# Kernel tuning notes

Measured on AMD Instinct MI355X. Metric: run time of the kernel, lower is better.

Reference implementation:

```python
import jax, jax.numpy as jnp
import numpy as np

C = 256
C8 = C // 8
B, H, W = 4, 64, 64


def setup_inputs() -> dict:
    key = jax.random.key(0)
    ks = jax.random.split(key, 8)
    s = 0.05
    return {
        "x": jax.random.normal(ks[0], (B, C, H, W), jnp.float32),
        "wq": jax.random.normal(ks[1], (C8, C), jnp.float32) * s,
        "bq": jax.random.normal(ks[2], (C8,), jnp.float32) * s,
        "wk": jax.random.normal(ks[3], (C8, C), jnp.float32) * s,
        "bk": jax.random.normal(ks[4], (C8,), jnp.float32) * s,
        "wv": jax.random.normal(ks[5], (C, C), jnp.float32) * s,
        "bv": jax.random.normal(ks[6], (C,), jnp.float32) * s,
        "gamma": jax.random.normal(ks[7], (1,), jnp.float32),
    }


def reference(x, wq, bq, wk, bk, wv, bv, gamma):
    b, c, h, w = x.shape
    n = h * w
    xf = x.reshape(b, c, n)                                   # [B,C,N]
    # 1x1 convs == channel matmuls
    q = jnp.einsum('dc,bcn->bnd', wq, xf) + bq                # [B,N,C8] (query, permuted)
    k = jnp.einsum('dc,bcn->bdn', wk, xf) + bk[None, :, None]  # [B,C8,N]
    v = jnp.einsum('ec,bcn->ben', wv, xf) + bv[None, :, None]  # [B,C,N]
    # attention[b,i,j] = <q_i, k_j>, softmax over j (no scaling, as in source)
    attn = jax.nn.softmax(jnp.einsum('bnd,bdm->bnm', q, k), axis=-1)  # [B,N,N]
    # out = value @ attn^T : out[b,e,i] = sum_j v[b,e,j] * attn[b,i,j]
    out = jnp.einsum('bej,bij->bei', v, attn).reshape(b, c, h, w)
    return gamma * out + x
```

## Files before the change

kernel.cpp:

```cpp
#include <hip/hip_runtime.h>
#include <math.h>

typedef __attribute__((ext_vector_type(8))) short bf16x8;
typedef __attribute__((ext_vector_type(4))) float f32x4;
typedef unsigned short ushort;
typedef unsigned int uint;

#define F4(p)  (*reinterpret_cast<float4*>(p))
#define CF4(p) (*reinterpret_cast<const float4*>(p))

__device__ __forceinline__ ushort f2bf(float f) {
    uint u = __float_as_uint(f);
    return (ushort)((u + 0x7FFFu + ((u >> 16) & 1u)) >> 16);
}
__device__ __forceinline__ float bf2f(ushort h) {
    return __uint_as_float(((uint)h) << 16);
}

__global__ __launch_bounds__(256) void proj_kernel(
    const float* __restrict__ x,
    const float* __restrict__ wq, const float* __restrict__ bq,
    const float* __restrict__ wk, const float* __restrict__ bk,
    const float* __restrict__ wv, const float* __restrict__ bv,
    ushort* __restrict__ ws)
{
    ushort* qth = ws;
    ushort* qtl = qth + 524288;
    ushort* kth = qtl + 524288;
    ushort* ktl = kth + 524288;
    ushort* vhp = ktl + 524288;
    ushort* vlp = vhp + 4194304;

    __shared__ float Xt[64][260];
    __shared__ __align__(16) ushort Oh[4096];
    __shared__ __align__(16) ushort Ol[4096];

    const int t   = threadIdx.x;
    const int blk = blockIdx.x;
    const int b   = blk >> 6;
    const int n0  = (blk & 63) * 64;

    {
        const int tn4 = (t & 15) * 4;
        const int c0  = t >> 4;
        #pragma unroll
        for (int cc = 0; cc < 16; ++cc) {
            const int c = c0 + (cc << 4);
            const float4 xv = CF4(&x[(((size_t)b * 256 + c) << 12) + n0 + tn4]);
            Xt[tn4 + 0][c] = xv.x;
            Xt[tn4 + 1][c] = xv.y;
            Xt[tn4 + 2][c] = xv.z;
            Xt[tn4 + 3][c] = xv.w;
        }
    }
    __syncthreads();

    const int td = t >> 4;
    const int tn = t & 15;

    for (int g = 0; g < 5; ++g) {
        const int d0 = g * 64;
        float acc[4][4];
        #pragma unroll
        for (int i = 0; i < 4; ++i)
            #pragma unroll
            for (int j = 0; j < 4; ++j) acc[i][j] = 0.f;

        const float* wrow[4];
        float bias[4];
        #pragma unroll
        for (int dd = 0; dd < 4; ++dd) {
            const int rr = d0 + td + (dd << 4);
            if (rr < 32)      { wrow[dd] = wq + rr * 256;        bias[dd] = bq[rr]; }
            else if (rr < 64) { wrow[dd] = wk + (rr - 32) * 256; bias[dd] = bk[rr - 32]; }
            else              { wrow[dd] = wv + (rr - 64) * 256; bias[dd] = bv[rr - 64]; }
        }

        for (int c = 0; c < 256; c += 4) {
            float4 w4[4];
            #pragma unroll
            for (int dd = 0; dd < 4; ++dd) w4[dd] = CF4(&wrow[dd][c]);
            #pragma unroll
            for (int nn = 0; nn < 4; ++nn) {
                const float4 xv = CF4(&Xt[tn + (nn << 4)][c]);
                #pragma unroll
                for (int dd = 0; dd < 4; ++dd) {
                    acc[dd][nn] += w4[dd].x * xv.x + w4[dd].y * xv.y
                                 + w4[dd].z * xv.z + w4[dd].w * xv.w;
                }
            }
        }

        #pragma unroll
        for (int dd = 0; dd < 4; ++dd) {
            const int rr = d0 + td + (dd << 4);
            #pragma unroll
            for (int nn = 0; nn < 4; ++nn) {
                const int nl  = tn + (nn << 4);
                const float val = acc[dd][nn] + bias[dd];
                const ushort h  = f2bf(val);
                const ushort lo = f2bf(val - bf2f(h));
                int o;
                if (g == 0) o = (rr < 32) ? nl * 32 + rr : 2048 + nl * 32 + (rr - 32);
                else        o = (rr - d0) * 64 + nl;
                Oh[o] = h; Ol[o] = lo;
            }
        }
        __syncthreads();

        if (g == 0) {
            const size_t qb = ((size_t)(b * 4096 + n0)) * 32;
            #pragma unroll
            for (int s = 0; s < 2; ++s) {
                const int o = t * 16 + s * 8;
                const float4 vh = F4(&Oh[o]);
                const float4 vl = F4(&Ol[o]);
                if (o < 2048) {
                    F4(&qth[qb + o]) = vh;
                    F4(&qtl[qb + o]) = vl;
                } else {
                    F4(&kth[qb + o - 2048]) = vh;
                    F4(&ktl[qb + o - 2048]) = vl;
                }
            }
        } else {
            const size_t vb = ((size_t)(b * 256 + (g - 1) * 64)) * 4096 + n0;
            #pragma unroll
            for (int s = 0; s < 2; ++s) {
                const int o  = t * 16 + s * 8;
                const size_t ga = vb + (size_t)(o >> 6) * 4096 + (o & 63);
                F4(&vhp[ga]) = F4(&Oh[o]);
                F4(&vlp[ga]) = F4(&Ol[o]);
            }
        }
        __syncthreads();
    }
}

__global__ __launch_bounds__(256, 2) void attn_kernel(
    const ushort* __restrict__ ws,
    const float* __restrict__ x,
    const float* __restrict__ gamma,
    float* __restrict__ out)
{
    const ushort* qth = ws;
    const ushort* qtl = qth + 524288;
    const ushort* kth = qtl + 524288;
    const ushort* ktl = kth + 524288;
    const ushort* vhp = ktl + 524288;
    const ushort* vlp = vhp + 4194304;

    __shared__ __align__(16) ushort Ph[4096];
    __shared__ __align__(16) ushort Pl[4096];
    __shared__ float fac_sh[64];
    __shared__ float l_sh[64];

    const int t    = threadIdx.x;
    const int w    = t >> 6;
    const int lane = t & 63;
    const int m    = lane & 15;
    const int gr   = lane >> 4;

    const int blk = blockIdx.x;
    const int e8  = blk & 7;
    const int g_  = blk >> 3;
    const int b   = e8 >> 1;
    const int i0  = ((g_ & 31) + ((e8 & 1) << 5)) << 6;
    const int ebase = ((g_ >> 5) << 7) + w * 32;

    const size_t qkbase = (size_t)b * 4096 * 32;
    const size_t vbase  = (size_t)b * 256 * 4096;

    const int iq = i0 + w * 16 + m;
    const bf16x8 qbh = *(const bf16x8*)(qth + qkbase + (size_t)iq * 32 + 8 * gr);
    const bf16x8 qbl = *(const bf16x8*)(qtl + qkbase + (size_t)iq * 32 + 8 * gr);

    f32x4 accv[2][4];
    #pragma unroll
    for (int a = 0; a < 2; ++a)
        #pragma unroll
        for (int c = 0; c < 4; ++c) accv[a][c] = f32x4{0.f, 0.f, 0.f, 0.f};

    float m_run = -INFINITY, l_run = 0.f;
    const int irow = w * 16 + m;

    for (int jt = 0; jt < 64; ++jt) {
        const int j0 = jt << 6;

        bf16x8 kh[4], kl[4];
        #pragma unroll
        for (int mf = 0; mf < 4; ++mf) {
            const size_t ko = qkbase + (size_t)(j0 + mf * 16 + m) * 32 + 8 * gr;
            kh[mf] = *(const bf16x8*)(kth + ko);
            kl[mf] = *(const bf16x8*)(ktl + ko);
        }
        f32x4 st[4];
        #pragma unroll
        for (int mf = 0; mf < 4; ++mf) {
            f32x4 a = {0.f, 0.f, 0.f, 0.f};
            a = __builtin_amdgcn_mfma_f32_16x16x32_bf16(kh[mf], qbh, a, 0, 0, 0);
            a = __builtin_amdgcn_mfma_f32_16x16x32_bf16(kh[mf], qbl, a, 0, 0, 0);
            a = __builtin_amdgcn_mfma_f32_16x16x32_bf16(kl[mf], qbh, a, 0, 0, 0);
            st[mf] = a;
        }
        float tm = st[0][0];
        #pragma unroll
        for (int mf = 0; mf < 4; ++mf)
            #pragma unroll
            for (int r = 0; r < 4; ++r) tm = fmaxf(tm, st[mf][r]);
        tm = fmaxf(tm, __shfl_xor(tm, 16));
        tm = fmaxf(tm, __shfl_xor(tm, 32));
        const float m_new = fmaxf(m_run, tm);
        const float fac   = __expf(m_run - m_new);
        float p[4][4];
        float ts = 0.f;
        #pragma unroll
        for (int mf = 0; mf < 4; ++mf)
            #pragma unroll
            for (int r = 0; r < 4; ++r) {
                p[mf][r] = __expf(st[mf][r] - m_new);
                ts += p[mf][r];
            }
        ts += __shfl_xor(ts, 16);
        ts += __shfl_xor(ts, 32);
        l_run = l_run * fac + ts;
        m_run = m_new;

        #pragma unroll
        for (int mf = 0; mf < 4; ++mf) {
            const int j    = mf * 16 + 4 * gr;
            const int addr = irow * 64 + (j ^ ((irow & 7) << 3));
            ushort h0 = f2bf(p[mf][0]), h1 = f2bf(p[mf][1]);
            ushort h2 = f2bf(p[mf][2]), h3 = f2bf(p[mf][3]);
            ushort l0 = f2bf(p[mf][0] - bf2f(h0)), l1 = f2bf(p[mf][1] - bf2f(h1));
            ushort l2 = f2bf(p[mf][2] - bf2f(h2)), l3 = f2bf(p[mf][3] - bf2f(h3));
            *reinterpret_cast<uint2*>(&Ph[addr]) =
                make_uint2((uint)h0 | ((uint)h1 << 16), (uint)h2 | ((uint)h3 << 16));
            *reinterpret_cast<uint2*>(&Pl[addr]) =
                make_uint2((uint)l0 | ((uint)l1 << 16), (uint)l2 | ((uint)l3 << 16));
        }
        if (gr == 0) fac_sh[irow] = fac;
        __syncthreads();

        float fc[4];
        #pragma unroll
        for (int f = 0; f < 4; ++f) fc[f] = fac_sh[f * 16 + m];
        #pragma unroll
        for (int mf = 0; mf < 2; ++mf)
            #pragma unroll
            for (int f = 0; f < 4; ++f)
                #pragma unroll
                for (int r = 0; r < 4; ++r) accv[mf][f][r] *= fc[f];

        #pragma unroll
        for (int ks = 0; ks < 2; ++ks) {
            bf16x8 pbh[4], pbl[4];
            #pragma unroll
            for (int f = 0; f < 4; ++f) {
                const int i_   = f * 16 + m;
                const int j    = ks * 32 + 8 * gr;
                const int addr = i_ * 64 + (j ^ ((i_ & 7) << 3));
                pbh[f] = *reinterpret_cast<const bf16x8*>(&Ph[addr]);
                pbl[f] = *reinterpret_cast<const bf16x8*>(&Pl[addr]);
            }
            #pragma unroll
            for (int mf = 0; mf < 2; ++mf) {
                const size_t vo = vbase + (size_t)(ebase + mf * 16 + m) * 4096
                                + j0 + ks * 32 + 8 * gr;
                const bf16x8 vah = *(const bf16x8*)(vhp + vo);
                const bf16x8 val = *(const bf16x8*)(vlp + vo);
                #pragma unroll
                for (int f = 0; f < 4; ++f) {
                    accv[mf][f] = __builtin_amdgcn_mfma_f32_16x16x32_bf16(vah, pbh[f], accv[mf][f], 0, 0, 0);
                    accv[mf][f] = __builtin_amdgcn_mfma_f32_16x16x32_bf16(vah, pbl[f], accv[mf][f], 0, 0, 0);
                    accv[mf][f] = __builtin_amdgcn_mfma_f32_16x16x32_bf16(val, pbh[f], accv[mf][f], 0, 0, 0);
                }
            }
        }
        __syncthreads();
    }

    if (gr == 0) l_sh[irow] = l_run;
    __syncthreads();

    const float gv = gamma[0];
    float sc[4];
    #pragma unroll
    for (int f = 0; f < 4; ++f) sc[f] = gv / l_sh[f * 16 + m];
    #pragma unroll
    for (int mf = 0; mf < 2; ++mf)
        #pragma unroll
        for (int f = 0; f < 4; ++f)
            #pragma unroll
            for (int r = 0; r < 4; ++r) {
                const int e = ebase + mf * 16 + 4 * gr + r;
                const int i = i0 + f * 16 + m;
                const size_t idx = ((size_t)b * 256 + e) * 4096 + i;
                out[idx] = accv[mf][f][r] * sc[f] + x[idx];
            }
}

extern "C" void kernel_launch(void* const* d_in, const int* in_sizes, int n_in,
                              void* d_out, int out_size, void* d_ws, size_t ws_size,
                              hipStream_t stream) {
    const float* x     = (const float*)d_in[0];
    const float* wq    = (const float*)d_in[1];
    const float* bq    = (const float*)d_in[2];
    const float* wk    = (const float*)d_in[3];
    const float* bk    = (const float*)d_in[4];
    const float* wv    = (const float*)d_in[5];
    const float* bv    = (const float*)d_in[6];
    const float* gamma = (const float*)d_in[7];
    float* out  = (float*)d_out;
    ushort* ws  = (ushort*)d_ws;

    proj_kernel<<<256, 256, 0, stream>>>(x, wq, bq, wk, bk, wv, bv, ws);
    attn_kernel<<<512, 256, 0, stream>>>(ws, x, gamma, out);
}
```

Baseline: 360.3 us.

## Shrink projection tiles, double-buffer P, prefetch K/V, use hardware bf16 packing

The projection kernel now processes 16 positions per block instead of 64 and launches 1024 blocks, giving each thread one column and so less register and LDS use per block. The attention kernel double-buffers the P and scale shared arrays so the trailing barrier can be dropped. It also issues the V loads at the start of each tile and prefetches the next K tile into registers, to hide global latency behind the softmax work. The f32-to-bf16 conversion switches to the HIP intrinsics, including a packed two-value conversion. The costs are higher register pressure in the attention kernel and lower arithmetic reuse per weight load in the projection kernel.

```diff
diff --git a/kernel.cpp b/kernel.cpp
--- a/kernel.cpp
+++ b/kernel.cpp
@@ -1,4 +1,5 @@
 #include <hip/hip_runtime.h>
+#include <hip/hip_bf16.h>
 #include <math.h>
 
 typedef __attribute__((ext_vector_type(8))) short bf16x8;
@@ -9,12 +10,16 @@
 #define F4(p)  (*reinterpret_cast<float4*>(p))
 #define CF4(p) (*reinterpret_cast<const float4*>(p))
 
-__device__ __forceinline__ ushort f2bf(float f) {
-    uint u = __float_as_uint(f);
-    return (ushort)((u + 0x7FFFu + ((u >> 16) & 1u)) >> 16);
-}
 __device__ __forceinline__ float bf2f(ushort h) {
     return __uint_as_float(((uint)h) << 16);
+}
+__device__ __forceinline__ ushort f2bf(float f) {
+    __hip_bfloat16 h = __float2bfloat16(f);
+    ushort u; __builtin_memcpy(&u, &h, 2); return u;
+}
+__device__ __forceinline__ uint packbf2(float a, float b) {
+    __hip_bfloat162 h2 = __float22bfloat162_rn(make_float2(a, b));
+    uint u; __builtin_memcpy(&u, &h2, 4); return u;
 }
 
 __global__ __launch_bounds__(256) void proj_kernel(
@@ -31,21 +36,21 @@
     ushort* vhp = ktl + 524288;
     ushort* vlp = vhp + 4194304;
 
-    __shared__ float Xt[64][260];
-    __shared__ __align__(16) ushort Oh[4096];
-    __shared__ __align__(16) ushort Ol[4096];
+    __shared__ float Xt[16][260];
+    __shared__ __align__(16) ushort Oh[1024];
+    __shared__ __align__(16) ushort Ol[1024];
 
     const int t   = threadIdx.x;
     const int blk = blockIdx.x;
-    const int b   = blk >> 6;
-    const int n0  = (blk & 63) * 64;
+    const int b   = blk >> 8;
+    const int n0  = (blk & 255) * 16;
 
     {
-        const int tn4 = (t & 15) * 4;
-        const int c0  = t >> 4;
-        #pragma unroll
-        for (int cc = 0; cc < 16; ++cc) {
-            const int c = c0 + (cc << 4);
+        const int tn4 = (t & 3) * 4;
+        const int c0  = t >> 2;
+        #pragma unroll
+        for (int p = 0; p < 4; ++p) {
+            const int c = c0 + (p << 6);
             const float4 xv = CF4(&x[(((size_t)b * 256 + c) << 12) + n0 + tn4]);
             Xt[tn4 + 0][c] = xv.x;
             Xt[tn4 + 1][c] = xv.y;
@@ -60,11 +65,7 @@
 
     for (int g = 0; g < 5; ++g) {
         const int d0 = g * 64;
-        float acc[4][4];
-        #pragma unroll
-        for (int i = 0; i < 4; ++i)
-            #pragma unroll
-            for (int j = 0; j < 4; ++j) acc[i][j] = 0.f;
+        float acc[4] = {0.f, 0.f, 0.f, 0.f};
 
         const float* wrow[4];
         float bias[4];
@@ -77,60 +78,45 @@
         }
 
         for (int c = 0; c < 256; c += 4) {
-            float4 w4[4];
-            #pragma unroll
-            for (int dd = 0; dd < 4; ++dd) w4[dd] = CF4(&wrow[dd][c]);
-            #pragma unroll
-            for (int nn = 0; nn < 4; ++nn) {
-                const float4 xv = CF4(&Xt[tn + (nn << 4)][c]);
-                #pragma unroll
-                for (int dd = 0; dd < 4; ++dd) {
-                    acc[dd][nn] += w4[dd].x * xv.x + w4[dd].y * xv.y
-                                 + w4[dd].z * xv.z + w4[dd].w * xv.w;
+            const float4 xv = CF4(&Xt[tn][c]);
+            #pragma unroll
+            for (int dd = 0; dd < 4; ++dd) {
+                const float4 w4 = CF4(&wrow[dd][c]);
+                acc[dd] += w4.x * xv.x + w4.y * xv.y + w4.z * xv.z + w4.w * xv.w;
+            }
+        }
+
+        #pragma unroll
+        for (int dd = 0; dd < 4; ++dd) {
+            const int rr  = d0 + td + (dd << 4);
+            const float val = acc[dd] + bias[dd];
+            const ushort h  = f2bf(val);
+            const ushort lo = f2bf(val - bf2f(h));
+            int o;
+            if (g == 0) o = (rr < 32) ? tn * 32 + rr : 512 + tn * 32 + (rr - 32);
+            else        o = (rr - d0) * 16 + tn;
+            Oh[o] = h; Ol[o] = lo;
+        }
+        __syncthreads();
+
+        {
+            const int o = t * 4;
+            const uint2 vh = *reinterpret_cast<uint2*>(&Oh[o]);
+            const uint2 vl = *reinterpret_cast<uint2*>(&Ol[o]);
+            if (g == 0) {
+                const size_t qb = ((size_t)(b * 4096 + n0)) * 32;
+                if (o < 512) {
+                    *reinterpret_cast<uint2*>(&qth[qb + o]) = vh;
+                    *reinterpret_cast<uint2*>(&qtl[qb + o]) = vl;
+                } else {
+                    *reinterpret_cast<uint2*>(&kth[qb + o - 512]) = vh;
+                    *reinterpret_cast<uint2*>(&ktl[qb + o - 512]) = vl;
                 }
-            }
-        }
-
-        #pragma unroll
-        for (int dd = 0; dd < 4; ++dd) {
-            const int rr = d0 + td + (dd << 4);
-            #pragma unroll
-            for (int nn = 0; nn < 4; ++nn) {
-                const int nl  = tn + (nn << 4);
-                const float val = acc[dd][nn] + bias[dd];
-                const ushort h  = f2bf(val);
-                const ushort lo = f2bf(val - bf2f(h));
-                int o;
-                if (g == 0) o = (rr < 32) ? nl * 32 + rr : 2048 + nl * 32 + (rr - 32);
-                else        o = (rr - d0) * 64 + nl;
-                Oh[o] = h; Ol[o] = lo;
-            }
-        }
-        __syncthreads();
-
-        if (g == 0) {
-            const size_t qb = ((size_t)(b * 4096 + n0)) * 32;
-            #pragma unroll
-            for (int s = 0; s < 2; ++s) {
-                const int o = t * 16 + s * 8;
-                const float4 vh = F4(&Oh[o]);
-                const float4 vl = F4(&Ol[o]);
-                if (o < 2048) {
-                    F4(&qth[qb + o]) = vh;
-                    F4(&qtl[qb + o]) = vl;
-                } else {
-                    F4(&kth[qb + o - 2048]) = vh;
-                    F4(&ktl[qb + o - 2048]) = vl;
-                }
-            }
-        } else {
-            const size_t vb = ((size_t)(b * 256 + (g - 1) * 64)) * 4096 + n0;
-            #pragma unroll
-            for (int s = 0; s < 2; ++s) {
-                const int o  = t * 16 + s * 8;
-                const size_t ga = vb + (size_t)(o >> 6) * 4096 + (o & 63);
-                F4(&vhp[ga]) = F4(&Oh[o]);
-                F4(&vlp[ga]) = F4(&Ol[o]);
+            } else {
+                const size_t vb = ((size_t)(b * 256 + (g - 1) * 64)) * 4096 + n0;
+                const size_t ga = vb + (size_t)(o >> 4) * 4096 + (o & 15);
+                *reinterpret_cast<uint2*>(&vhp[ga]) = vh;
+                *reinterpret_cast<uint2*>(&vlp[ga]) = vl;
             }
         }
         __syncthreads();
@@ -150,9 +136,9 @@
     const ushort* vhp = ktl + 524288;
     const ushort* vlp = vhp + 4194304;
 
-    __shared__ __align__(16) ushort Ph[4096];
-    __shared__ __align__(16) ushort Pl[4096];
-    __shared__ float fac_sh[64];
+    __shared__ __align__(16) ushort Ph[2][4096];
+    __shared__ __align__(16) ushort Pl[2][4096];
+    __shared__ float fac_sh[2][64];
     __shared__ float l_sh[64];
 
     const int t    = threadIdx.x;
@@ -184,16 +170,29 @@
     float m_run = -INFINITY, l_run = 0.f;
     const int irow = w * 16 + m;
 
+    bf16x8 kh[4], kl[4];
+    #pragma unroll
+    for (int mf = 0; mf < 4; ++mf) {
+        const size_t ko = qkbase + (size_t)(mf * 16 + m) * 32 + 8 * gr;
+        kh[mf] = *(const bf16x8*)(kth + ko);
+        kl[mf] = *(const bf16x8*)(ktl + ko);
+    }
+
     for (int jt = 0; jt < 64; ++jt) {
-        const int j0 = jt << 6;
-
-        bf16x8 kh[4], kl[4];
-        #pragma unroll
-        for (int mf = 0; mf < 4; ++mf) {
-            const size_t ko = qkbase + (size_t)(j0 + mf * 16 + m) * 32 + 8 * gr;
-            kh[mf] = *(const bf16x8*)(kth + ko);
-            kl[mf] = *(const bf16x8*)(ktl + ko);
-        }
+        const int j0  = jt << 6;
+        const int buf = jt & 1;
+
+        bf16x8 vh_r[4], vl_r[4];
+        #pragma unroll
+        for (int ks = 0; ks < 2; ++ks)
+            #pragma unroll
+            for (int mf = 0; mf < 2; ++mf) {
+                const size_t vo = vbase + (size_t)(ebase + mf * 16 + m) * 4096
+                                + j0 + ks * 32 + 8 * gr;
+                vh_r[ks * 2 + mf] = *(const bf16x8*)(vhp + vo);
+                vl_r[ks * 2 + mf] = *(const bf16x8*)(vlp + vo);
+            }
+
         f32x4 st[4];
         #pragma unroll
         for (int mf = 0; mf < 4; ++mf) {
@@ -203,6 +202,7 @@
             a = __builtin_amdgcn_mfma_f32_16x16x32_bf16(kl[mf], qbh, a, 0, 0, 0);
             st[mf] = a;
         }
+
         float tm = st[0][0];
         #pragma unroll
         for (int mf = 0; mf < 4; ++mf)
@@ -230,21 +230,32 @@
         for (int mf = 0; mf < 4; ++mf) {
             const int j    = mf * 16 + 4 * gr;
             const int addr = irow * 64 + (j ^ ((irow & 7) << 3));
-            ushort h0 = f2bf(p[mf][0]), h1 = f2bf(p[mf][1]);
-            ushort h2 = f2bf(p[mf][2]), h3 = f2bf(p[mf][3]);
-            ushort l0 = f2bf(p[mf][0] - bf2f(h0)), l1 = f2bf(p[mf][1] - bf2f(h1));
-            ushort l2 = f2bf(p[mf][2] - bf2f(h2)), l3 = f2bf(p[mf][3] - bf2f(h3));
-            *reinterpret_cast<uint2*>(&Ph[addr]) =
-                make_uint2((uint)h0 | ((uint)h1 << 16), (uint)h2 | ((uint)h3 << 16));
-            *reinterpret_cast<uint2*>(&Pl[addr]) =
-                make_uint2((uint)l0 | ((uint)l1 << 16), (uint)l2 | ((uint)l3 << 16));
-        }
-        if (gr == 0) fac_sh[irow] = fac;
+            const uint h01 = packbf2(p[mf][0], p[mf][1]);
+            const uint h23 = packbf2(p[mf][2], p[mf][3]);
+            const float r0 = p[mf][0] - bf2f((ushort)h01);
+            const float r1 = p[mf][1] - bf2f((ushort)(h01 >> 16));
+            const float r2 = p[mf][2] - bf2f((ushort)h23);
+            const float r3 = p[mf][3] - bf2f((ushort)(h23 >> 16));
+            *reinterpret_cast<uint2*>(&Ph[buf][addr]) = make_uint2(h01, h23);
+            *reinterpret_cast<uint2*>(&Pl[buf][addr]) =
+                make_uint2(packbf2(r0, r1), packbf2(r2, r3));
+        }
+        if (gr == 0) fac_sh[buf][irow] = fac;
+
+        const int jn0 = ((jt + 1) & 63) << 6;
+        bf16x8 kh_n[4], kl_n[4];
+        #pragma unroll
+        for (int mf = 0; mf < 4; ++mf) {
+            const size_t ko = qkbase + (size_t)(jn0 + mf * 16 + m) * 32 + 8 * gr;
+            kh_n[mf] = *(const bf16x8*)(kth + ko);
+            kl_n[mf] = *(const bf16x8*)(ktl + ko);
+        }
+
         __syncthreads();
 
         float fc[4];
         #pragma unroll
-        for (int f = 0; f < 4; ++f) fc[f] = fac_sh[f * 16 + m];
+        for (int f = 0; f < 4; ++f) fc[f] = fac_sh[buf][f * 16 + m];
         #pragma unroll
         for (int mf = 0; mf < 2; ++mf)
             #pragma unroll
@@ -260,15 +271,13 @@
                 const int i_   = f * 16 + m;
                 const int j    = ks * 32 + 8 * gr;
                 const int addr = i_ * 64 + (j ^ ((i_ & 7) << 3));
-                pbh[f] = *reinterpret_cast<const bf16x8*>(&Ph[addr]);
-                pbl[f] = *reinterpret_cast<const bf16x8*>(&Pl[addr]);
+                pbh[f] = *reinterpret_cast<const bf16x8*>(&Ph[buf][addr]);
+                pbl[f] = *reinterpret_cast<const bf16x8*>(&Pl[buf][addr]);
             }
             #pragma unroll
             for (int mf = 0; mf < 2; ++mf) {
-                const size_t vo = vbase + (size_t)(ebase + mf * 16 + m) * 4096
-                                + j0 + ks * 32 + 8 * gr;
-                const bf16x8 vah = *(const bf16x8*)(vhp + vo);
-                const bf16x8 val = *(const bf16x8*)(vlp + vo);
+                const bf16x8 vah = vh_r[ks * 2 + mf];
+                const bf16x8 val = vl_r[ks * 2 + mf];
                 #pragma unroll
                 for (int f = 0; f < 4; ++f) {
                     accv[mf][f] = __builtin_amdgcn_mfma_f32_16x16x32_bf16(vah, pbh[f], accv[mf][f], 0, 0, 0);
@@ -277,7 +286,9 @@
                 }
             }
         }
-        __syncthreads();
+
+        #pragma unroll
+        for (int mf = 0; mf < 4; ++mf) { kh[mf] = kh_n[mf]; kl[mf] = kl_n[mf]; }
     }
 
     if (gr == 0) l_sh[irow] = l_run;
@@ -314,6 +325,6 @@
     float* out  = (float*)d_out;
     ushort* ws  = (ushort*)d_ws;
 
-    proj_kernel<<<256, 256, 0, stream>>>(x, wq, bq, wk, bk, wv, bv, ws);
+    proj_kernel<<<1024, 256, 0, stream>>>(x, wq, bq, wk, bk, wv, bv, ws);
     attn_kernel<<<512, 256, 0, stream>>>(ws, x, gamma, out);
 }
```

Measured after the change: 406.9 us. 1.13x slower.
